# Performance work log

Hardware: AMD Instinct MI355X
Metric: run time of the kernel (lower is better)

Reference implementation:

```python
import jax, jax.numpy as jnp
import numpy as np

N = 20000      # nodes
E = 320000     # edges (before self-loops)
IN, HID, H, OUT = 128, 256, 4, 64
NEG_SLOPE = 0.2


def setup_inputs() -> dict:
    key = jax.random.key(0)
    ks = jax.random.split(key, 2 + 4 * 4)
    inp = {
        "x": jax.random.normal(ks[0], (N, IN), dtype=jnp.float32),
        "edge_index": jax.random.randint(ks[1], (2, E), 0, N, dtype=jnp.int32),
    }
    # (d_in, heads, channels) per layer; last layer heads=1, concat=False
    dims = [(IN, H, HID), (H * HID, H, HID), (H * HID, H, HID), (H * HID, 1, OUT)]
    for i, (din, h, c) in enumerate(dims):
        k = ks[2 + 4 * i: 6 + 4 * i]
        glorot = (2.0 / (din + h * c)) ** 0.5
        inp[f"W{i}"] = jax.random.normal(k[0], (din, h * c), jnp.float32) * glorot
        inp[f"a_src{i}"] = jax.random.normal(k[1], (h, c), jnp.float32) * 0.1
        inp[f"a_dst{i}"] = jax.random.normal(k[2], (h, c), jnp.float32) * 0.1
        inp[f"b{i}"] = jnp.zeros((h * c,), jnp.float32)
    return inp


def _gat_conv(x, src, dst, W, a_src, a_dst, b, concat):
    heads, ch = a_src.shape
    h = (x @ W).reshape(N, heads, ch)                       # [N,H,C]
    alpha_s = jnp.einsum('nhc,hc->nh', h, a_src)            # [N,H]
    alpha_d = jnp.einsum('nhc,hc->nh', h, a_dst)
    e = jax.nn.leaky_relu(alpha_s[src] + alpha_d[dst], NEG_SLOPE)  # [Etot,H]
    # segment softmax over incoming edges of each destination node
    m = jax.ops.segment_max(e, dst, num_segments=N)
    ex = jnp.exp(e - m[dst])
    denom = jax.ops.segment_sum(ex, dst, num_segments=N)
    alpha = ex / (denom[dst] + 1e-16)                       # [Etot,H]
    msg = h[src] * alpha[:, :, None]                        # [Etot,H,C]
    out = jax.ops.segment_sum(msg, dst, num_segments=N)     # [N,H,C]
    out = out.reshape(N, heads * ch) if concat else out.mean(axis=1)
    return out + b


def reference(x, edge_index,
              W0, a_src0, a_dst0, b0,
              W1, a_src1, a_dst1, b1,
              W2, a_src2, a_dst2, b2,
              W3, a_src3, a_dst3, b3):
    # PyG GATConv adds self-loops by default
    loops = jnp.arange(N, dtype=edge_index.dtype)
    src = jnp.concatenate([edge_index[0], loops])
    dst = jnp.concatenate([edge_index[1], loops])
    params = [(W0, a_src0, a_dst0, b0), (W1, a_src1, a_dst1, b1),
              (W2, a_src2, a_dst2, b2), (W3, a_src3, a_dst3, b3)]
    hcur = x
    for i in range(3):
        hcur = _gat_conv(hcur, src, dst, *params[i], concat=True)
        hcur = jax.nn.elu(hcur)          # dropout is identity in eval mode
    return _gat_conv(hcur, src, dst, *params[3], concat=False)
```

## Files before the change

kernel.cpp:

```cpp
#include <hip/hip_runtime.h>
#include <math.h>

#define IN_DIM 128
#define OUT_DIM 64

typedef __attribute__((ext_vector_type(8))) _Float16 f16x8;
typedef __attribute__((ext_vector_type(4))) float f32x4;
typedef __attribute__((ext_vector_type(4))) _Float16 half4;

#define WSCALE 32.0f
#define WINV   (1.0f / 32.0f)

__device__ __forceinline__ void async_copy16(void* lds, const void* g) {
    __builtin_amdgcn_global_load_lds(
        (const __attribute__((address_space(1))) unsigned int*)g,
        (__attribute__((address_space(3))) unsigned int*)lds, 16, 0, 0);
}

__global__ void count_deg_kernel(const int* __restrict__ dst, int* __restrict__ deg, int e) {
    int i = blockIdx.x * blockDim.x + threadIdx.x;
    if (i < e) atomicAdd(&deg[dst[i]], 1);
}

__global__ __launch_bounds__(1024)
void scan_offsets_kernel(const int* __restrict__ deg, int* __restrict__ offs, int n) {
    __shared__ int partial[1024];
    const int tid = threadIdx.x;
    const int chunk = (n + 1023) / 1024;
    const int lo = tid * chunk;
    const int hi = min(lo + chunk, n);
    int s = 0;
    for (int i = lo; i < hi; ++i) s += deg[i];
    partial[tid] = s;
    __syncthreads();
    for (int d = 1; d < 1024; d <<= 1) {
        int v = (tid >= d) ? partial[tid - d] : 0;
        __syncthreads();
        partial[tid] += v;
        __syncthreads();
    }
    int run = (tid == 0) ? 0 : partial[tid - 1];
    for (int i = lo; i < hi; ++i) { offs[i] = run; run += deg[i]; }
    if (hi == n) offs[n] = run;
}

__global__ void scatter_edges_kernel(const int* __restrict__ src, const int* __restrict__ dst,
                                     const int* __restrict__ offs, int* __restrict__ cursor,
                                     int* __restrict__ esrc, int e) {
    int i = blockIdx.x * blockDim.x + threadIdx.x;
    if (i < e) {
        int d = dst[i];
        int pos = offs[d] + atomicAdd(&cursor[d], 1);
        esrc[pos] = src[i];
    }
}

__global__ void x_to_f16_kernel(const float* __restrict__ x, _Float16* __restrict__ out, size_t n4) {
    size_t i = (size_t)blockIdx.x * blockDim.x + threadIdx.x;
    if (i >= n4) return;
    float4 v = *(const float4*)&x[i * 4];
    half4 h;
    h[0] = (_Float16)v.x; h[1] = (_Float16)v.y; h[2] = (_Float16)v.z; h[3] = (_Float16)v.w;
    *(half4*)&out[i * 4] = h;
}

__global__ __launch_bounds__(256)
void transpose_f16(const float* __restrict__ W, _Float16* __restrict__ out,
                   int K, int Nc) {
    __shared__ float t[32][33];
    const int k0 = blockIdx.x * 32, n0 = blockIdx.y * 32;
    const int tx = threadIdx.x, ty = threadIdx.y;
    #pragma unroll
    for (int j = 0; j < 32; j += 8)
        t[ty + j][tx] = W[(size_t)(k0 + ty + j) * Nc + n0 + tx];
    __syncthreads();
    #pragma unroll
    for (int j = 0; j < 32; j += 8)
        out[(size_t)(n0 + ty + j) * K + k0 + tx] = (_Float16)(t[tx][ty + j] * WSCALE);
}

__global__ __launch_bounds__(256, 2)
void gemm_f16_mfma(const _Float16* __restrict__ A, const _Float16* __restrict__ Wt,
                   float* __restrict__ C, _Float16* __restrict__ C16,
                   int Nc, int K, size_t hstride16,
                   const float* __restrict__ Asrc, const float* __restrict__ Adst,
                   float* __restrict__ as_out, float* __restrict__ ad_out, int Nrows) {
    __shared__ char smem[65536];

    const int tid = threadIdx.x;
    const int w = tid >> 6;
    const int lane = tid & 63;
    const int wr = w >> 1, wc = w & 1;
    const int bcol = blockIdx.x * 128;
    const int brow = blockIdx.y * 128;

    const size_t rb = (size_t)K * 2;

    int rr[4], bs[4], ldso[4];
    #pragma unroll
    for (int i = 0; i < 4; ++i) {
        int d = w * 4096 + i * 1024 + lane * 16;
        ldso[i] = d;
        rr[i] = d >> 7;
        bs[i] = (d & 127) ^ ((rr[i] & 7) << 4);
    }

    const char* gA = (const char*)A  + (size_t)brow * rb;
    const char* gB = (const char*)Wt + (size_t)bcol * rb;

    f32x4 acc[4][4];
    #pragma unroll
    for (int i = 0; i < 4; ++i)
        #pragma unroll
        for (int j = 0; j < 4; ++j) acc[i][j] = (f32x4)0.f;

    #pragma unroll
    for (int i = 0; i < 4; ++i) {
        const size_t goff = (size_t)rr[i] * rb + bs[i];
        async_copy16(smem + ldso[i],         gA + goff);
        async_copy16(smem + 16384 + ldso[i], gB + goff);
    }
    __syncthreads();

    int cur = 0;
    for (int k0 = 0; k0 < K; k0 += 64) {
        if (k0 + 64 < K) {
            char* dA = smem + (cur ^ 1) * 32768;
            char* dB = dA + 16384;
            const size_t kb = (size_t)(k0 + 64) * 2;
            #pragma unroll
            for (int i = 0; i < 4; ++i) {
                const size_t goff = (size_t)rr[i] * rb + kb + bs[i];
                async_copy16(dA + ldso[i], gA + goff);
                async_copy16(dB + ldso[i], gB + goff);
            }
        }

        const char* sA = smem + cur * 32768;
        const char* sB = sA + 16384;
        #pragma unroll
        for (int kk = 0; kk < 2; ++kk) {
            f16x8 a[4], b[4];
            const int kbyte = kk * 64 + ((lane >> 4) * 16);
            #pragma unroll
            for (int f = 0; f < 4; ++f) {
                const int ra = wr * 64 + f * 16 + (lane & 15);
                a[f] = *(const f16x8*)(sA + ra * 128 + (kbyte ^ ((ra & 7) << 4)));
                const int rbn = wc * 64 + f * 16 + (lane & 15);
                b[f] = *(const f16x8*)(sB + rbn * 128 + (kbyte ^ ((rbn & 7) << 4)));
            }
            #pragma unroll
            for (int m = 0; m < 4; ++m)
                #pragma unroll
                for (int n = 0; n < 4; ++n)
                    acc[m][n] = __builtin_amdgcn_mfma_f32_16x16x32_f16(a[m], b[n], acc[m][n], 0, 0, 0);
        }

        __syncthreads();
        cur ^= 1;
    }

    #pragma unroll
    for (int m = 0; m < 4; ++m)
        #pragma unroll
        for (int n = 0; n < 4; ++n) acc[m][n] *= WINV;

    const int rowb = brow + wr * 64 + ((lane >> 4) * 4);
    const int colb = bcol + wc * 64 + (lane & 15);
    if (C16) {
        #pragma unroll
        for (int m = 0; m < 4; ++m)
            #pragma unroll
            for (int n = 0; n < 4; ++n) {
                const int col = colb + n * 16;
                const size_t base = (size_t)(col >> 8) * hstride16 + (size_t)(col & 255);
                #pragma unroll
                for (int j = 0; j < 4; ++j)
                    C16[base + (size_t)(rowb + m * 16 + j) * 256] = (_Float16)acc[m][n][j];
            }
        if (as_out) {
            const int lcol = lane & 15;
            const int cb = bcol + wc * 64;
            const int head = cb >> 8;
            float as4[4], ad4[4];
            #pragma unroll
            for (int n = 0; n < 4; ++n) {
                as4[n] = Asrc[cb + n * 16 + lcol];
                ad4[n] = Adst[cb + n * 16 + lcol];
            }
            #pragma unroll
            for (int m = 0; m < 4; ++m)
                #pragma unroll
                for (int j = 0; j < 4; ++j) {
                    float ps = acc[m][0][j] * as4[0] + acc[m][1][j] * as4[1]
                             + acc[m][2][j] * as4[2] + acc[m][3][j] * as4[3];
                    float pd = acc[m][0][j] * ad4[0] + acc[m][1][j] * ad4[1]
                             + acc[m][2][j] * ad4[2] + acc[m][3][j] * ad4[3];
                    #pragma unroll
                    for (int o = 1; o < 16; o <<= 1) {
                        ps += __shfl_xor(ps, o);
                        pd += __shfl_xor(pd, o);
                    }
                    if (lcol == 0) {
                        const int row = rowb + m * 16 + j;
                        if (row < Nrows) {
                            atomicAdd(&as_out[(size_t)head * Nrows + row], ps);
                            atomicAdd(&ad_out[(size_t)head * Nrows + row], pd);
                        }
                    }
                }
        }
    } else {
        #pragma unroll
        for (int m = 0; m < 4; ++m)
            #pragma unroll
            for (int n = 0; n < 4; ++n) {
                const int col = colb + n * 16;
                if (col < Nc) {
                    #pragma unroll
                    for (int j = 0; j < 4; ++j)
                        C[(size_t)(rowb + m * 16 + j) * Nc + col] = acc[m][n][j];
                }
            }
    }
}

__global__ void alpha32_kernel(const float* __restrict__ h, const float* __restrict__ a_src,
                               const float* __restrict__ a_dst,
                               float* __restrict__ as_out, float* __restrict__ ad_out, int N) {
    const int n = blockIdx.x;
    const int lane = threadIdx.x;
    float v = h[(size_t)n * 64 + lane];
    float ss = v * a_src[lane];
    float sd = v * a_dst[lane];
    #pragma unroll
    for (int o = 32; o > 0; o >>= 1) { ss += __shfl_down(ss, o); sd += __shfl_down(sd, o); }
    if (lane == 0) {
        as_out[n] = ss;
        ad_out[n] = sd;
    }
}

__global__ __launch_bounds__(64)
void spmm16_kernel(const _Float16* __restrict__ h,
                   const float* __restrict__ as_,
                   const float* __restrict__ ad_,
                   const int* __restrict__ offs, const int* __restrict__ esrc,
                   const float* __restrict__ bias,
                   int N, int hm,
                   _Float16* __restrict__ out16) {
    const int n = blockIdx.x;
    const int w = blockIdx.y;
    const int lane = threadIdx.x;

    const _Float16* hw = h + (size_t)w * hm * 256;
    const float* asw = as_ + (size_t)w * N;
    const float ad  = ad_[(size_t)w * N + n];

    float e0 = asw[n] + ad;
    e0 = (e0 > 0.f) ? e0 : 0.2f * e0;
    const int lo = offs[n], hi = offs[n + 1];

    float sum;
    float acc0, acc1, acc2, acc3;
    {
        const float p0 = __expf(e0);
        sum = p0;
        half4 t = *(const half4*)(hw + (size_t)n * 256 + lane * 4);
        acc0 = p0 * (float)t[0]; acc1 = p0 * (float)t[1];
        acc2 = p0 * (float)t[2]; acc3 = p0 * (float)t[3];
    }

    int j = lo;
    for (; j + 4 <= hi; j += 4) {
        const int s0 = esrc[j], s1 = esrc[j + 1], s2 = esrc[j + 2], s3 = esrc[j + 3];
        const half4 r0 = *(const half4*)(hw + (size_t)s0 * 256 + lane * 4);
        const half4 r1 = *(const half4*)(hw + (size_t)s1 * 256 + lane * 4);
        const half4 r2 = *(const half4*)(hw + (size_t)s2 * 256 + lane * 4);
        const half4 r3 = *(const half4*)(hw + (size_t)s3 * 256 + lane * 4);
        float e, p0, p1, p2, p3;
        e = asw[s0] + ad; e = (e > 0.f) ? e : 0.2f * e; p0 = __expf(e);
        e = asw[s1] + ad; e = (e > 0.f) ? e : 0.2f * e; p1 = __expf(e);
        e = asw[s2] + ad; e = (e > 0.f) ? e : 0.2f * e; p2 = __expf(e);
        e = asw[s3] + ad; e = (e > 0.f) ? e : 0.2f * e; p3 = __expf(e);
        sum += (p0 + p1) + (p2 + p3);
        acc0 += p0 * (float)r0[0] + p1 * (float)r1[0] + p2 * (float)r2[0] + p3 * (float)r3[0];
        acc1 += p0 * (float)r0[1] + p1 * (float)r1[1] + p2 * (float)r2[1] + p3 * (float)r3[1];
        acc2 += p0 * (float)r0[2] + p1 * (float)r1[2] + p2 * (float)r2[2] + p3 * (float)r3[2];
        acc3 += p0 * (float)r0[3] + p1 * (float)r1[3] + p2 * (float)r2[3] + p3 * (float)r3[3];
    }
    for (; j < hi; ++j) {
        const int s = esrc[j];
        float e = asw[s] + ad;
        e = (e > 0.f) ? e : 0.2f * e;
        const float p = __expf(e);
        sum += p;
        half4 t = *(const half4*)(hw + (size_t)s * 256 + lane * 4);
        acc0 += p * (float)t[0]; acc1 += p * (float)t[1];
        acc2 += p * (float)t[2]; acc3 += p * (float)t[3];
    }

    const float inv = 1.0f / (sum + 1e-16f);
    float v0 = acc0 * inv + bias[w * 256 + lane * 4 + 0];
    float v1 = acc1 * inv + bias[w * 256 + lane * 4 + 1];
    float v2 = acc2 * inv + bias[w * 256 + lane * 4 + 2];
    float v3 = acc3 * inv + bias[w * 256 + lane * 4 + 3];
    v0 = (v0 > 0.f) ? v0 : (__expf(v0) - 1.0f);
    v1 = (v1 > 0.f) ? v1 : (__expf(v1) - 1.0f);
    v2 = (v2 > 0.f) ? v2 : (__expf(v2) - 1.0f);
    v3 = (v3 > 0.f) ? v3 : (__expf(v3) - 1.0f);

    half4 hv;
    hv[0] = (_Float16)v0; hv[1] = (_Float16)v1;
    hv[2] = (_Float16)v2; hv[3] = (_Float16)v3;
    *(half4*)&out16[(size_t)n * 1024 + (size_t)w * 256 + lane * 4] = hv;
}

__global__ __launch_bounds__(64)
void spmm32_kernel(const float* __restrict__ h,
                   const float* __restrict__ as_, const float* __restrict__ ad_,
                   const int* __restrict__ offs, const int* __restrict__ esrc,
                   const float* __restrict__ bias,
                   int N, float* __restrict__ out) {
    const int n = blockIdx.x;
    const int lane = threadIdx.x;

    const float ad  = ad_[n];
    float e0 = as_[n] + ad;
    e0 = (e0 > 0.f) ? e0 : 0.2f * e0;
    const int lo = offs[n], hi = offs[n + 1];

    float sum;
    float acc;
    {
        const float p0 = __expf(e0);
        sum = p0;
        acc = p0 * h[(size_t)n * 64 + lane];
    }

    int j = lo;
    for (; j + 4 <= hi; j += 4) {
        const int s0 = esrc[j], s1 = esrc[j + 1], s2 = esrc[j + 2], s3 = esrc[j + 3];
        const float r0 = h[(size_t)s0 * 64 + lane];
        const float r1 = h[(size_t)s1 * 64 + lane];
        const float r2 = h[(size_t)s2 * 64 + lane];
        const float r3 = h[(size_t)s3 * 64 + lane];
        float e, p0, p1, p2, p3;
        e = as_[s0] + ad; e = (e > 0.f) ? e : 0.2f * e; p0 = __expf(e);
        e = as_[s1] + ad; e = (e > 0.f) ? e : 0.2f * e; p1 = __expf(e);
        e = as_[s2] + ad; e = (e > 0.f) ? e : 0.2f * e; p2 = __expf(e);
        e = as_[s3] + ad; e = (e > 0.f) ? e : 0.2f * e; p3 = __expf(e);
        sum += (p0 + p1) + (p2 + p3);
        acc += p0 * r0 + p1 * r1 + p2 * r2 + p3 * r3;
    }
    for (; j < hi; ++j) {
        const int s = esrc[j];
        float e = as_[s] + ad;
        e = (e > 0.f) ? e : 0.2f * e;
        const float p = __expf(e);
        sum += p;
        acc += p * h[(size_t)s * 64 + lane];
    }

    out[(size_t)n * 64 + lane] = acc / (sum + 1e-16f) + bias[lane];
}

extern "C" void kernel_launch(void* const* d_in, const int* in_sizes, int n_in,
                              void* d_out, int out_size, void* d_ws, size_t ws_size,
                              hipStream_t stream) {
    const float* x    = (const float*)d_in[0];
    const int*   edge = (const int*)d_in[1];
    const int N = in_sizes[0] / IN_DIM;
    const int E = in_sizes[1] / 2;
    const int Mp = ((N + 127) / 128) * 128;

    const float* W[4]; const float* As[4]; const float* Ad[4]; const float* Bb[4];
    for (int i = 0; i < 4; ++i) {
        W[i]  = (const float*)d_in[2 + 4 * i];
        As[i] = (const float*)d_in[3 + 4 * i];
        Ad[i] = (const float*)d_in[4 + 4 * i];
        Bb[i] = (const float*)d_in[5 + 4 * i];
    }

    char* ws = (char*)d_ws;
    auto alloc = [&](size_t bytes) {
        char* p = ws;
        ws += (bytes + 255) & ~(size_t)255;
        return p;
    };
    _Float16*  h16   = (_Float16*)alloc((size_t)4 * Mp * 256 * 2);
    _Float16*  X16   = (_Float16*)alloc((size_t)Mp * 1024 * 2);
    float*     bufA  = (float*)alloc((size_t)Mp * OUT_DIM * 4);
    _Float16*  Wt    = (_Float16*)alloc((size_t)1024 * 1024 * 2);
    float*     as_buf = (float*)alloc((size_t)N * 4 * 4);
    float*     ad_buf = (float*)alloc((size_t)N * 4 * 4);
    int*       deg    = (int*)alloc((size_t)(N + 1) * 4);
    int*       offs   = (int*)alloc((size_t)(N + 1) * 4);
    int*       cursor = (int*)alloc((size_t)N * 4);
    int*       esrc   = (int*)alloc((size_t)E * 4);
    (void)ws_size;

    const int* e_src = edge;
    const int* e_dst = edge + E;

    hipMemsetAsync(deg, 0, (size_t)N * 4, stream);
    count_deg_kernel<<<(E + 255) / 256, 256, 0, stream>>>(e_dst, deg, E);
    scan_offsets_kernel<<<1, 1024, 0, stream>>>(deg, offs, N);
    hipMemsetAsync(cursor, 0, (size_t)N * 4, stream);
    scatter_edges_kernel<<<(E + 255) / 256, 256, 0, stream>>>(e_src, e_dst, offs, cursor, esrc, E);

    hipMemsetAsync((char*)X16 + (size_t)N * 256, 0, (size_t)(Mp - N) * 256, stream);
    hipMemsetAsync((char*)X16 + (size_t)N * 2048, 0, (size_t)(Mp - N) * 2048, stream);

    {
        size_t n4 = (size_t)N * IN_DIM / 4;
        x_to_f16_kernel<<<(unsigned)((n4 + 255) / 256), 256, 0, stream>>>(x, X16, n4);
    }

    const dim3 tblk(32, 8);
    const int gx = Mp / 128;
    const size_t hstride16 = (size_t)Mp * 256;
    const size_t abytes = (size_t)N * 4 * 4;

    transpose_f16<<<dim3(IN_DIM / 32, 1024 / 32), tblk, 0, stream>>>(W[0], Wt, IN_DIM, 1024);
    hipMemsetAsync(as_buf, 0, abytes, stream);
    hipMemsetAsync(ad_buf, 0, abytes, stream);
    gemm_f16_mfma<<<dim3(8, gx), 256, 0, stream>>>(X16, Wt, nullptr, h16, 1024, IN_DIM, hstride16,
                                                   As[0], Ad[0], as_buf, ad_buf, N);
    spmm16_kernel<<<dim3(N, 4), 64, 0, stream>>>(
        h16, as_buf, ad_buf, offs, esrc, Bb[0], N, Mp, X16);

    for (int l = 1; l <= 2; ++l) {
        transpose_f16<<<dim3(1024 / 32, 1024 / 32), tblk, 0, stream>>>(W[l], Wt, 1024, 1024);
        hipMemsetAsync(as_buf, 0, abytes, stream);
        hipMemsetAsync(ad_buf, 0, abytes, stream);
        gemm_f16_mfma<<<dim3(8, gx), 256, 0, stream>>>(X16, Wt, nullptr, h16, 1024, 1024, hstride16,
                                                       As[l], Ad[l], as_buf, ad_buf, N);
        spmm16_kernel<<<dim3(N, 4), 64, 0, stream>>>(
            h16, as_buf, ad_buf, offs, esrc, Bb[l], N, Mp, X16);
    }

    hipMemsetAsync(Wt, 0, (size_t)128 * 1024 * 2, stream);
    transpose_f16<<<dim3(1024 / 32, OUT_DIM / 32), tblk, 0, stream>>>(W[3], Wt, 1024, OUT_DIM);
    gemm_f16_mfma<<<dim3(1, gx), 256, 0, stream>>>(X16, Wt, bufA, nullptr, OUT_DIM, 1024, 0,
                                                   nullptr, nullptr, nullptr, nullptr, N);
    alpha32_kernel<<<N, 64, 0, stream>>>(bufA, As[3], Ad[3], as_buf, ad_buf, N);
    spmm32_kernel<<<N, 64, 0, stream>>>(
        bufA, as_buf, ad_buf, offs, esrc, Bb[3], N, (float*)d_out);
}
```

Before: 529.1 us.

## Precompute per-edge attention weights in separate kernel and fuse final-layer alpha into GEMM

Result: slower. 553.7 us (+4.6%).

```diff
diff --git a/kernel.cpp b/kernel.cpp
--- a/kernel.cpp
+++ b/kernel.cpp
@@ -46,13 +46,25 @@
 
 __global__ void scatter_edges_kernel(const int* __restrict__ src, const int* __restrict__ dst,
                                      const int* __restrict__ offs, int* __restrict__ cursor,
-                                     int* __restrict__ esrc, int e) {
+                                     int* __restrict__ esrc, int* __restrict__ edst, int e) {
     int i = blockIdx.x * blockDim.x + threadIdx.x;
     if (i < e) {
         int d = dst[i];
         int pos = offs[d] + atomicAdd(&cursor[d], 1);
         esrc[pos] = src[i];
-    }
+        edst[pos] = d;
+    }
+}
+
+__global__ void edge_weights_kernel(const float* __restrict__ as_, const float* __restrict__ ad_,
+                                    const int* __restrict__ esrc, const int* __restrict__ edst,
+                                    int N, int E, float* __restrict__ pw) {
+    int j = blockIdx.x * blockDim.x + threadIdx.x;
+    if (j >= E) return;
+    const int w = blockIdx.y;
+    float e = as_[(size_t)w * N + esrc[j]] + ad_[(size_t)w * N + edst[j]];
+    e = (e > 0.f) ? e : 0.2f * e;
+    pw[(size_t)w * E + j] = __expf(e);
 }
 
 __global__ void x_to_f16_kernel(const float* __restrict__ x, _Float16* __restrict__ out, size_t n4) {
@@ -178,38 +190,6 @@
                 for (int j = 0; j < 4; ++j)
                     C16[base + (size_t)(rowb + m * 16 + j) * 256] = (_Float16)acc[m][n][j];
             }
-        if (as_out) {
-            const int lcol = lane & 15;
-            const int cb = bcol + wc * 64;
-            const int head = cb >> 8;
-            float as4[4], ad4[4];
-            #pragma unroll
-            for (int n = 0; n < 4; ++n) {
-                as4[n] = Asrc[cb + n * 16 + lcol];
-                ad4[n] = Adst[cb + n * 16 + lcol];
-            }
-            #pragma unroll
-            for (int m = 0; m < 4; ++m)
-                #pragma unroll
-                for (int j = 0; j < 4; ++j) {
-                    float ps = acc[m][0][j] * as4[0] + acc[m][1][j] * as4[1]
-                             + acc[m][2][j] * as4[2] + acc[m][3][j] * as4[3];
-                    float pd = acc[m][0][j] * ad4[0] + acc[m][1][j] * ad4[1]
-                             + acc[m][2][j] * ad4[2] + acc[m][3][j] * ad4[3];
-                    #pragma unroll
-                    for (int o = 1; o < 16; o <<= 1) {
-                        ps += __shfl_xor(ps, o);
-                        pd += __shfl_xor(pd, o);
-                    }
-                    if (lcol == 0) {
-                        const int row = rowb + m * 16 + j;
-                        if (row < Nrows) {
-                            atomicAdd(&as_out[(size_t)head * Nrows + row], ps);
-                            atomicAdd(&ad_out[(size_t)head * Nrows + row], pd);
-                        }
-                    }
-                }
-        }
     } else {
         #pragma unroll
         for (int m = 0; m < 4; ++m)
@@ -223,21 +203,38 @@
                 }
             }
     }
-}
-
-__global__ void alpha32_kernel(const float* __restrict__ h, const float* __restrict__ a_src,
-                               const float* __restrict__ a_dst,
-                               float* __restrict__ as_out, float* __restrict__ ad_out, int N) {
-    const int n = blockIdx.x;
-    const int lane = threadIdx.x;
-    float v = h[(size_t)n * 64 + lane];
-    float ss = v * a_src[lane];
-    float sd = v * a_dst[lane];
-    #pragma unroll
-    for (int o = 32; o > 0; o >>= 1) { ss += __shfl_down(ss, o); sd += __shfl_down(sd, o); }
-    if (lane == 0) {
-        as_out[n] = ss;
-        ad_out[n] = sd;
+
+    const int cb = bcol + wc * 64;
+    if (as_out && cb < Nc) {
+        const int lcol = lane & 15;
+        const int head = cb >> 8;
+        float as4[4], ad4[4];
+        #pragma unroll
+        for (int n = 0; n < 4; ++n) {
+            as4[n] = Asrc[cb + n * 16 + lcol];
+            ad4[n] = Adst[cb + n * 16 + lcol];
+        }
+        #pragma unroll
+        for (int m = 0; m < 4; ++m)
+            #pragma unroll
+            for (int j = 0; j < 4; ++j) {
+                float ps = acc[m][0][j] * as4[0] + acc[m][1][j] * as4[1]
+                         + acc[m][2][j] * as4[2] + acc[m][3][j] * as4[3];
+                float pd = acc[m][0][j] * ad4[0] + acc[m][1][j] * ad4[1]
+                         + acc[m][2][j] * ad4[2] + acc[m][3][j] * ad4[3];
+                #pragma unroll
+                for (int o = 1; o < 16; o <<= 1) {
+                    ps += __shfl_xor(ps, o);
+                    pd += __shfl_xor(pd, o);
+                }
+                if (lcol == 0) {
+                    const int row = rowb + m * 16 + j;
+                    if (row < Nrows) {
+                        atomicAdd(&as_out[(size_t)head * Nrows + row], ps);
+                        atomicAdd(&ad_out[(size_t)head * Nrows + row], pd);
+                    }
+                }
+            }
     }
 }
 
@@ -245,57 +242,66 @@
 void spmm16_kernel(const _Float16* __restrict__ h,
                    const float* __restrict__ as_,
                    const float* __restrict__ ad_,
+                   const float* __restrict__ pw,
                    const int* __restrict__ offs, const int* __restrict__ esrc,
                    const float* __restrict__ bias,
-                   int N, int hm,
+                   int N, int hm, int E,
                    _Float16* __restrict__ out16) {
     const int n = blockIdx.x;
     const int w = blockIdx.y;
     const int lane = threadIdx.x;
 
-    const _Float16* hw = h + (size_t)w * hm * 256;
-    const float* asw = as_ + (size_t)w * N;
-    const float ad  = ad_[(size_t)w * N + n];
-
-    float e0 = asw[n] + ad;
-    e0 = (e0 > 0.f) ? e0 : 0.2f * e0;
+    const _Float16* hl = h + (size_t)w * hm * 256 + lane * 4;
+    const float* pww = pw + (size_t)w * E;
     const int lo = offs[n], hi = offs[n + 1];
 
     float sum;
     float acc0, acc1, acc2, acc3;
     {
+        float e0 = as_[(size_t)w * N + n] + ad_[(size_t)w * N + n];
+        e0 = (e0 > 0.f) ? e0 : 0.2f * e0;
         const float p0 = __expf(e0);
         sum = p0;
-        half4 t = *(const half4*)(hw + (size_t)n * 256 + lane * 4);
+        half4 t = *(const half4*)(hl + (size_t)n * 256);
         acc0 = p0 * (float)t[0]; acc1 = p0 * (float)t[1];
         acc2 = p0 * (float)t[2]; acc3 = p0 * (float)t[3];
     }
 
     int j = lo;
+    for (; j + 8 <= hi; j += 8) {
+        int s[8]; float p[8]; half4 r[8];
+        #pragma unroll
+        for (int q = 0; q < 8; ++q) { s[q] = esrc[j + q]; p[q] = pww[j + q]; }
+        #pragma unroll
+        for (int q = 0; q < 8; ++q) r[q] = *(const half4*)(hl + (size_t)s[q] * 256);
+        #pragma unroll
+        for (int q = 0; q < 8; ++q) {
+            sum  += p[q];
+            acc0 += p[q] * (float)r[q][0];
+            acc1 += p[q] * (float)r[q][1];
+            acc2 += p[q] * (float)r[q][2];
+            acc3 += p[q] * (float)r[q][3];
+        }
+    }
     for (; j + 4 <= hi; j += 4) {
-        const int s0 = esrc[j], s1 = esrc[j + 1], s2 = esrc[j + 2], s3 = esrc[j + 3];
-        const half4 r0 = *(const half4*)(hw + (size_t)s0 * 256 + lane * 4);
-        const half4 r1 = *(const half4*)(hw + (size_t)s1 * 256 + lane * 4);
-        const half4 r2 = *(const half4*)(hw + (size_t)s2 * 256 + lane * 4);
-        const half4 r3 = *(const half4*)(hw + (size_t)s3 * 256 + lane * 4);
-        float e, p0, p1, p2, p3;
-        e = asw[s0] + ad; e = (e > 0.f) ? e : 0.2f * e; p0 = __expf(e);
-        e = asw[s1] + ad; e = (e > 0.f) ? e : 0.2f * e; p1 = __expf(e);
-        e = asw[s2] + ad; e = (e > 0.f) ? e : 0.2f * e; p2 = __expf(e);
-        e = asw[s3] + ad; e = (e > 0.f) ? e : 0.2f * e; p3 = __expf(e);
-        sum += (p0 + p1) + (p2 + p3);
-        acc0 += p0 * (float)r0[0] + p1 * (float)r1[0] + p2 * (float)r2[0] + p3 * (float)r3[0];
-        acc1 += p0 * (float)r0[1] + p1 * (float)r1[1] + p2 * (float)r2[1] + p3 * (float)r3[1];
-        acc2 += p0 * (float)r0[2] + p1 * (float)r1[2] + p2 * (float)r2[2] + p3 * (float)r3[2];
-        acc3 += p0 * (float)r0[3] + p1 * (float)r1[3] + p2 * (float)r2[3] + p3 * (float)r3[3];
+        int s[4]; float p[4]; half4 r[4];
+        #pragma unroll
+        for (int q = 0; q < 4; ++q) { s[q] = esrc[j + q]; p[q] = pww[j + q]; }
+        #pragma unroll
+        for (int q = 0; q < 4; ++q) r[q] = *(const half4*)(hl + (size_t)s[q] * 256);
+        #pragma unroll
+        for (int q = 0; q < 4; ++q) {
+            sum  += p[q];
+            acc0 += p[q] * (float)r[q][0];
+            acc1 += p[q] * (float)r[q][1];
+            acc2 += p[q] * (float)r[q][2];
+            acc3 += p[q] * (float)r[q][3];
+        }
     }
     for (; j < hi; ++j) {
-        const int s = esrc[j];
-        float e = asw[s] + ad;
-        e = (e > 0.f) ? e : 0.2f * e;
-        const float p = __expf(e);
-        sum += p;
-        half4 t = *(const half4*)(hw + (size_t)s * 256 + lane * 4);
+        const float p = pww[j];
+        half4 t = *(const half4*)(hl + (size_t)esrc[j] * 256);
+        sum  += p;
         acc0 += p * (float)t[0]; acc1 += p * (float)t[1];
         acc2 += p * (float)t[2]; acc3 += p * (float)t[3];
     }
@@ -319,20 +325,18 @@
 __global__ __launch_bounds__(64)
 void spmm32_kernel(const float* __restrict__ h,
                    const float* __restrict__ as_, const float* __restrict__ ad_,
+                   const float* __restrict__ pw,
                    const int* __restrict__ offs, const int* __restrict__ esrc,
                    const float* __restrict__ bias,
                    int N, float* __restrict__ out) {
     const int n = blockIdx.x;
     const int lane = threadIdx.x;
-
-    const float ad  = ad_[n];
-    float e0 = as_[n] + ad;
-    e0 = (e0 > 0.f) ? e0 : 0.2f * e0;
     const int lo = offs[n], hi = offs[n + 1];
 
-    float sum;
-    float acc;
+    float sum, acc;
     {
+        float e0 = as_[n] + ad_[n];
+        e0 = (e0 > 0.f) ? e0 : 0.2f * e0;
         const float p0 = __expf(e0);
         sum = p0;
         acc = p0 * h[(size_t)n * 64 + lane];
@@ -340,26 +344,18 @@
 
     int j = lo;
     for (; j + 4 <= hi; j += 4) {
-        const int s0 = esrc[j], s1 = esrc[j + 1], s2 = esrc[j + 2], s3 = esrc[j + 3];
-        const float r0 = h[(size_t)s0 * 64 + lane];
-        const float r1 = h[(size_t)s1 * 64 + lane];
-        const float r2 = h[(size_t)s2 * 64 + lane];
-        const float r3 = h[(size_t)s3 * 64 + lane];
-        float e, p0, p1, p2, p3;
-        e = as_[s0] + ad; e = (e > 0.f) ? e : 0.2f * e; p0 = __expf(e);
-        e = as_[s1] + ad; e = (e > 0.f) ? e : 0.2f * e; p1 = __expf(e);
-        e = as_[s2] + ad; e = (e > 0.f) ? e : 0.2f * e; p2 = __expf(e);
-        e = as_[s3] + ad; e = (e > 0.f) ? e : 0.2f * e; p3 = __expf(e);
-        sum += (p0 + p1) + (p2 + p3);
-        acc += p0 * r0 + p1 * r1 + p2 * r2 + p3 * r3;
+        int s[4]; float p[4]; float r[4];
+        #pragma unroll
+        for (int q = 0; q < 4; ++q) { s[q] = esrc[j + q]; p[q] = pw[j + q]; }
+        #pragma unroll
+        for (int q = 0; q < 4; ++q) r[q] = h[(size_t)s[q] * 64 + lane];
+        #pragma unroll
+        for (int q = 0; q < 4; ++q) { sum += p[q]; acc += p[q] * r[q]; }
     }
     for (; j < hi; ++j) {
-        const int s = esrc[j];
-        float e = as_[s] + ad;
-        e = (e > 0.f) ? e : 0.2f * e;
-        const float p = __expf(e);
+        const float p = pw[j];
         sum += p;
-        acc += p * h[(size_t)s * 64 + lane];
+        acc += p * h[(size_t)esrc[j] * 64 + lane];
     }
 
     out[(size_t)n * 64 + lane] = acc / (sum + 1e-16f) + bias[lane];
@@ -392,12 +388,14 @@
     _Float16*  X16   = (_Float16*)alloc((size_t)Mp * 1024 * 2);
     float*     bufA  = (float*)alloc((size_t)Mp * OUT_DIM * 4);
     _Float16*  Wt    = (_Float16*)alloc((size_t)1024 * 1024 * 2);
+    float*     pw    = (float*)alloc((size_t)4 * E * 4);
     float*     as_buf = (float*)alloc((size_t)N * 4 * 4);
     float*     ad_buf = (float*)alloc((size_t)N * 4 * 4);
     int*       deg    = (int*)alloc((size_t)(N + 1) * 4);
     int*       offs   = (int*)alloc((size_t)(N + 1) * 4);
     int*       cursor = (int*)alloc((size_t)N * 4);
     int*       esrc   = (int*)alloc((size_t)E * 4);
+    int*       edst   = (int*)alloc((size_t)E * 4);
     (void)ws_size;
 
     const int* e_src = edge;
@@ -407,7 +405,7 @@
     count_deg_kernel<<<(E + 255) / 256, 256, 0, stream>>>(e_dst, deg, E);
     scan_offsets_kernel<<<1, 1024, 0, stream>>>(deg, offs, N);
     hipMemsetAsync(cursor, 0, (size_t)N * 4, stream);
-    scatter_edges_kernel<<<(E + 255) / 256, 256, 0, stream>>>(e_src, e_dst, offs, cursor, esrc, E);
+    scatter_edges_kernel<<<(E + 255) / 256, 256, 0, stream>>>(e_src, e_dst, offs, cursor, esrc, edst, E);
 
     hipMemsetAsync((char*)X16 + (size_t)N * 256, 0, (size_t)(Mp - N) * 256, stream);
     hipMemsetAsync((char*)X16 + (size_t)N * 2048, 0, (size_t)(Mp - N) * 2048, stream);
@@ -419,6 +417,7 @@
 
     const dim3 tblk(32, 8);
     const int gx = Mp / 128;
+    const int egx = (E + 255) / 256;
     const size_t hstride16 = (size_t)Mp * 256;
     const size_t abytes = (size_t)N * 4 * 4;
 
@@ -427,8 +426,9 @@
     hipMemsetAsync(ad_buf, 0, abytes, stream);
     gemm_f16_mfma<<<dim3(8, gx), 256, 0, stream>>>(X16, Wt, nullptr, h16, 1024, IN_DIM, hstride16,
                                                    As[0], Ad[0], as_buf, ad_buf, N);
+    edge_weights_kernel<<<dim3(egx, 4), 256, 0, stream>>>(as_buf, ad_buf, esrc, edst, N, E, pw);
     spmm16_kernel<<<dim3(N, 4), 64, 0, stream>>>(
-        h16, as_buf, ad_buf, offs, esrc, Bb[0], N, Mp, X16);
+        h16, as_buf, ad_buf, pw, offs, esrc, Bb[0], N, Mp, E, X16);
 
     for (int l = 1; l <= 2; ++l) {
         transpose_f16<<<dim3(1024 / 32, 1024 / 32), tblk, 0, stream>>>(W[l], Wt, 1024, 1024);
@@ -436,15 +436,18 @@
         hipMemsetAsync(ad_buf, 0, abytes, stream);
         gemm_f16_mfma<<<dim3(8, gx), 256, 0, stream>>>(X16, Wt, nullptr, h16, 1024, 1024, hstride16,
                                                        As[l], Ad[l], as_buf, ad_buf, N);
+        edge_weights_kernel<<<dim3(egx, 4), 256, 0, stream>>>(as_buf, ad_buf, esrc, edst, N, E, pw);
         spmm16_kernel<<<dim3(N, 4), 64, 0, stream>>>(
-            h16, as_buf, ad_buf, offs, esrc, Bb[l], N, Mp, X16);
+            h16, as_buf, ad_buf, pw, offs, esrc, Bb[l], N, Mp, E, X16);
     }
 
     hipMemsetAsync(Wt, 0, (size_t)128 * 1024 * 2, stream);
     transpose_f16<<<dim3(1024 / 32, OUT_DIM / 32), tblk, 0, stream>>>(W[3], Wt, 1024, OUT_DIM);
+    hipMemsetAsync(as_buf, 0, abytes, stream);
+    hipMemsetAsync(ad_buf, 0, abytes, stream);
     gemm_f16_mfma<<<dim3(1, gx), 256, 0, stream>>>(X16, Wt, bufA, nullptr, OUT_DIM, 1024, 0,
-                                                   nullptr, nullptr, nullptr, nullptr, N);
-    alpha32_kernel<<<N, 64, 0, stream>>>(bufA, As[3], Ad[3], as_buf, ad_buf, N);
+                                                   As[3], Ad[3], as_buf, ad_buf, N);
+    edge_weights_kernel<<<dim3(egx, 1), 256, 0, stream>>>(as_buf, ad_buf, esrc, edst, N, E, pw);
     spmm32_kernel<<<N, 64, 0, stream>>>(
-        bufA, as_buf, ad_buf, offs, esrc, Bb[3], N, (float*)d_out);
-}
+        bufA, as_buf, ad_buf, pw, offs, esrc, Bb[3], N, (float*)d_out);
+}
```
